# Kernel tuning notes

Measured on AMD Instinct MI355X. Metric: run time of the kernel, lower is better.

The kernel has to match this reference:

```python
import jax, jax.numpy as jnp
import numpy as np


def _conv1x1_relu(x, W, b):
    # x: (B, Cin, N, k), W: (Cout, Cin), b: (Cout,) -> (B, Cout, N, k)
    return jax.nn.relu(jnp.einsum('bcnk,oc->bonk', x, W) + b[None, :, None, None])


def _knn_idx(pc, k):
    # pc: (B, C, N). Mirrors torch: dis_mat = -||pi - pj||^2, topk (largest) -> nearest.
    G = jnp.einsum('bcn,bcm->bnm', pc, pc)            # (B, N, N)
    sq = jnp.sum(pc * pc, axis=1)                      # (B, N)
    neg_dist = 2.0 * G - sq[:, :, None] - sq[:, None, :]
    _, idx = jax.lax.top_k(neg_dist, k)                # (B, N, k) int32
    return idx


def _group_points(x, idx):
    # x: (B, C, N), idx: (B, N, k) -> (B, C, N, k); out[b,c,n,j] = x[b,c,idx[b,n,j]]
    B, C, N = x.shape
    k = idx.shape[-1]
    idx2 = jnp.broadcast_to(idx.reshape(B, 1, N * k), (B, C, N * k))
    return jnp.take_along_axis(x, idx2, axis=2).reshape(B, C, N, k)


def setup_inputs() -> dict:
    key = jax.random.key(0)
    ks = jax.random.split(key, 8)
    B, N, C, O, K = 8, 4096, 64, 64, 16
    s = 0.05
    return {
        'xyz': jax.random.normal(ks[0], (B, 3, N), dtype=jnp.float32),
        'fea': jax.random.normal(ks[1], (B, C, N), dtype=jnp.float32),
        'Wg1': jax.random.normal(ks[2], (O, 10), dtype=jnp.float32) * s,
        'bg1': jnp.zeros((O,), dtype=jnp.float32),
        'Wg2': jax.random.normal(ks[3], (O, O), dtype=jnp.float32) * s,
        'bg2': jnp.zeros((O,), dtype=jnp.float32),
        'Wf1': jax.random.normal(ks[4], (O, 2 * C), dtype=jnp.float32) * s,
        'bf1': jnp.zeros((O,), dtype=jnp.float32),
        'Wf2': jax.random.normal(ks[5], (O, O), dtype=jnp.float32) * s,
        'bf2': jnp.zeros((O,), dtype=jnp.float32),
        'Wf3': jax.random.normal(ks[6], (O, O), dtype=jnp.float32) * s,
        'bf3': jnp.zeros((O,), dtype=jnp.float32),
        'k': 16,
    }


def reference(xyz, fea, Wg1, bg1, Wg2, bg2, Wf1, bf1, Wf2, bf2, Wf3, bf3, k):
    idx = _knn_idx(fea, k)                             # (B, N, k)

    # get_edge_point: (B, 10, N, k)
    xyz_knn = _group_points(xyz, idx)                  # (B, 3, N, k)
    xyz_c = jnp.broadcast_to(xyz[:, :, :, None], xyz_knn.shape)
    xyz_r = xyz_c - xyz_knn
    xyz_d = jnp.sqrt(jnp.sum(xyz_r * xyz_r, axis=1, keepdims=True))
    geo = jnp.concatenate([xyz_d, xyz_c, xyz_knn, xyz_r], axis=1)

    # get_edge_feature: (B, 2C, N, k)
    fea_knn = _group_points(fea, idx)
    fea_c = jnp.broadcast_to(fea[:, :, :, None], fea_knn.shape)
    edge = jnp.concatenate([fea_c, fea_knn], axis=1)

    g = _conv1x1_relu(geo, Wg1, bg1)
    g = _conv1x1_relu(g, Wg2, bg2)

    f = _conv1x1_relu(edge, Wf1, bf1)
    f = _conv1x1_relu(f, Wf2, bf2)
    f = _conv1x1_relu(f, Wf3, bf3)

    out = jnp.max(g * f, axis=-1)                      # (B, O, N)
    return out
```

## Files before the change

### kernel.cpp

```cpp
#include <hip/hip_runtime.h>
#include <math.h>

#define NB 8
#define NPTS 4096
#define NCH 64
#define NOUT 64
#define KNN 16

#define GLOBAL_AS const __attribute__((address_space(1)))
#define LDS_AS __attribute__((address_space(3)))

#define WS_SQ  0
#define WS_PT  (NB*NPTS)
#define WS_QT  (WS_PT + NB*NPTS*64)
#define WS_IDX (WS_QT + NB*NPTS*64)

__global__ __launch_bounds__(256) void k_sq(const float* __restrict__ fea,
                                            float* __restrict__ sq) {
    int g = blockIdx.x * 256 + threadIdx.x;
    int b = g >> 12, n = g & 4095;
    const float* f = fea + (size_t)b * NCH * NPTS + n;
    float s = 0.f;
#pragma unroll
    for (int c = 0; c < NCH; ++c) s = fmaf(f[c * NPTS], f[c * NPTS], s);
    sq[g] = s;
}

__global__ __launch_bounds__(256, 2) void k_knn(const float* __restrict__ fea,
                                                const float* __restrict__ sq,
                                                int* __restrict__ idxout) {
    __shared__ __align__(16) float rowT[64][64];
    __shared__ __align__(16) float colT[2][64 * 64];
    __shared__ __align__(16) float D[64 * 64];

    const int b = blockIdx.y;
    const int n0 = blockIdx.x * 64;
    const int tid = threadIdx.x;
    const int to = tid & 15, tp = tid >> 4;
    const int lane = tid & 63, w = tid >> 6;
    const int g = lane >> 4, p = lane & 15;
    const int wbase = w * 16;
    const float* feab = fea + (size_t)b * NCH * NPTS;

    auto stage_async = [&](int buf, int m0) {
#pragma unroll
        for (int i = 0; i < 4; ++i) {
            int k = w * 4 + i;
            int c = 4 * k + (lane >> 4);
            int j = (lane & 15) * 4;
            const float* gp = feab + c * NPTS + m0 + j;
            float* lp = &colT[buf][k * 256];
            __builtin_amdgcn_global_load_lds((GLOBAL_AS void*)gp,
                                             (LDS_AS void*)lp, 16, 0, 0);
        }
    };

#pragma unroll
    for (int i = 0; i < 4; ++i) {
        int e = i * 1024 + tid * 4;
        int c = e >> 6, r = e & 63;
        *(float4*)&rowT[c][r] = *(const float4*)&feab[c * NPTS + n0 + r];
    }
    stage_async(0, 0);

    float lstv[4];
    int   lsti[4];
#pragma unroll
    for (int i = 0; i < 4; ++i) { lstv[i] = -3.0e38f; lsti[i] = 0; }

    auto ins = [&](int i, float vv, int col) {
        unsigned long long lt = __ballot(lstv[i] < vv);
        int pos = __popc((unsigned)((lt >> (g * 16)) & 0xFFFFull));
        float nv = __shfl_down(lstv[i], 1, 16);
        int   ni = __shfl_down(lsti[i], 1, 16);
        if (p <= pos - 2)      { lstv[i] = nv; lsti[i] = ni; }
        else if (p == pos - 1) { lstv[i] = vv; lsti[i] = col; }
    };

    __syncthreads();

    for (int t = 0; t < 64; ++t) {
        const int m0 = t * 64;
        const int cur = t & 1;
        if (t < 63) stage_async(cur ^ 1, m0 + 64);

        float4 sqc = *(const float4*)&sq[b * NPTS + m0 + tp * 4];

        float acc[4][4] = {{0.f,0.f,0.f,0.f},{0.f,0.f,0.f,0.f},
                           {0.f,0.f,0.f,0.f},{0.f,0.f,0.f,0.f}};
#pragma unroll 8
        for (int c = 0; c < 64; ++c) {
            float4 rv = *(const float4*)&rowT[c][to * 4];
            float4 cv = *(const float4*)&colT[cur][c * 64 + tp * 4];
            float rr[4] = {rv.x, rv.y, rv.z, rv.w};
            float cc[4] = {cv.x, cv.y, cv.z, cv.w};
#pragma unroll
            for (int ri = 0; ri < 4; ++ri)
#pragma unroll
                for (int ci = 0; ci < 4; ++ci)
                    acc[ri][ci] = fmaf(rr[ri], cc[ci], acc[ri][ci]);
        }

        float sqa[4] = {sqc.x, sqc.y, sqc.z, sqc.w};
#pragma unroll
        for (int ri = 0; ri < 4; ++ri) {
            int row = to * 4 + ri;
            int colp = (tp * 4) ^ (((row >> 2) & 15) << 2);
            float4 o;
            o.x = 2.f * acc[ri][0] - sqa[0];
            o.y = 2.f * acc[ri][1] - sqa[1];
            o.z = 2.f * acc[ri][2] - sqa[2];
            o.w = 2.f * acc[ri][3] - sqa[3];
            *(float4*)&D[row * 64 + colp] = o;
        }
        asm volatile("s_waitcnt lgkmcnt(0)\n\ts_barrier" ::: "memory");

        float4 dv[4];
        float thr[4];
#pragma unroll
        for (int i = 0; i < 4; ++i) {
            int row = wbase + g * 4 + i;
            int swz = ((row >> 2) & 15) << 2;
            dv[i] = *(const float4*)&D[row * 64 + ((p * 4) ^ swz)];
            thr[i] = __shfl(lstv[i], 0, 16);
        }
#pragma unroll
        for (int i = 0; i < 4; ++i) {
            float vm = fmaxf(fmaxf(dv[i].x, dv[i].y), fmaxf(dv[i].z, dv[i].w));
            unsigned long long bal = __ballot(vm > thr[i]);
            unsigned mg = (unsigned)((bal >> (g * 16)) & 0xFFFFull);
            while (__any(mg != 0u)) {
                bool act = (mg != 0u);
                int srcp = act ? (__ffs(mg) - 1) : 0;
                mg &= (mg - 1u);
                int srcl = (g << 4) | srcp;
                float c0 = __shfl(dv[i].x, srcl);
                float c1 = __shfl(dv[i].y, srcl);
                float c2 = __shfl(dv[i].z, srcl);
                float c3 = __shfl(dv[i].w, srcl);
                if (act) {
                    int cb = m0 + srcp * 4;
                    if (c0 > thr[i]) ins(i, c0, cb + 0);
                    if (c1 > thr[i]) ins(i, c1, cb + 1);
                    if (c2 > thr[i]) ins(i, c2, cb + 2);
                    if (c3 > thr[i]) ins(i, c3, cb + 3);
                }
            }
        }
        __syncthreads();
    }

#pragma unroll
    for (int i = 0; i < 4; ++i) {
        int row = wbase + g * 4 + i;
        idxout[((size_t)(b * NPTS) + n0 + row) * KNN + (15 - p)] = lsti[i];
    }
}

__global__ __launch_bounds__(256) void k_pq(const float* __restrict__ fea,
                                            const float* __restrict__ Wf1,
                                            const float* __restrict__ bf1,
                                            float* __restrict__ Pt,
                                            float* __restrict__ Qt) {
    __shared__ __align__(16) float feaT[64][64];
    __shared__ __align__(16) float WT[64][132];
    __shared__ float sb[64];

    const int b = blockIdx.y;
    const int n0 = blockIdx.x * 64;
    const int tid = threadIdx.x;
    const int to = tid & 15, tn = tid >> 4;
    const float* feab = fea + (size_t)b * NCH * NPTS;

#pragma unroll
    for (int i = 0; i < 4; ++i) {
        int e = i * 1024 + tid * 4;
        int c = e >> 6, nn = e & 63;
        *(float4*)&feaT[c][nn] = *(const float4*)&feab[c * NPTS + n0 + nn];
    }
#pragma unroll
    for (int i = 0; i < 8; ++i) {
        int g = tid * 32 + i * 4;
        int op = g >> 6, c = g & 63;
        const float* src = (op < 64) ? &Wf1[op * 128 + c]
                                     : &Wf1[(op - 64) * 128 + 64 + c];
        float4 w = *(const float4*)src;
        WT[c + 0][op] = w.x; WT[c + 1][op] = w.y;
        WT[c + 2][op] = w.z; WT[c + 3][op] = w.w;
    }
    if (tid < 64) sb[tid] = bf1[tid];
    __syncthreads();

    float acc[4][8];
#pragma unroll
    for (int ni = 0; ni < 4; ++ni)
#pragma unroll
        for (int oj = 0; oj < 8; ++oj) acc[ni][oj] = 0.f;

#pragma unroll 4
    for (int c = 0; c < 64; ++c) {
        float4 a  = *(const float4*)&feaT[c][tn * 4];
        float4 w0 = *(const float4*)&WT[c][to * 8];
        float4 w1 = *(const float4*)&WT[c][to * 8 + 4];
        float av[4] = {a.x, a.y, a.z, a.w};
        float wv[8] = {w0.x, w0.y, w0.z, w0.w, w1.x, w1.y, w1.z, w1.w};
#pragma unroll
        for (int ni = 0; ni < 4; ++ni)
#pragma unroll
            for (int oj = 0; oj < 8; ++oj)
                acc[ni][oj] = fmaf(av[ni], wv[oj], acc[ni][oj]);
    }

    const int opb = to * 8;
#pragma unroll
    for (int ni = 0; ni < 4; ++ni) {
        int n = n0 + tn * 4 + ni;
        size_t base = ((size_t)b * NPTS + n) * 64;
        if (opb < 64) {
            float4 o0, o1;
            o0.x = acc[ni][0] + sb[opb + 0]; o0.y = acc[ni][1] + sb[opb + 1];
            o0.z = acc[ni][2] + sb[opb + 2]; o0.w = acc[ni][3] + sb[opb + 3];
            o1.x = acc[ni][4] + sb[opb + 4]; o1.y = acc[ni][5] + sb[opb + 5];
            o1.z = acc[ni][6] + sb[opb + 6]; o1.w = acc[ni][7] + sb[opb + 7];
            *(float4*)&Pt[base + opb]     = o0;
            *(float4*)&Pt[base + opb + 4] = o1;
        } else {
            float4 o0, o1;
            o0.x = acc[ni][0]; o0.y = acc[ni][1]; o0.z = acc[ni][2]; o0.w = acc[ni][3];
            o1.x = acc[ni][4]; o1.y = acc[ni][5]; o1.z = acc[ni][6]; o1.w = acc[ni][7];
            *(float4*)&Qt[base + opb - 64]     = o0;
            *(float4*)&Qt[base + opb - 64 + 4] = o1;
        }
    }
}

__global__ __launch_bounds__(256) void k_mlp(
    const float* __restrict__ xyz,
    const float* __restrict__ Pt, const float* __restrict__ Qt,
    const int* __restrict__ knnidx,
    const float* __restrict__ Wg1, const float* __restrict__ bg1,
    const float* __restrict__ Wg2, const float* __restrict__ bg2,
    const float* __restrict__ Wf2, const float* __restrict__ bf2,
    const float* __restrict__ Wf3, const float* __restrict__ bf3,
    float* __restrict__ out) {
    __shared__ __align__(16) float bufX[64][68];
    __shared__ __align__(16) float bufY[64][68];
    __shared__ __align__(16) float Wbuf[64][68];
    __shared__ __align__(16) float scratch[1280];
    __shared__ float biasS[64];
    __shared__ int sidx[64];

    const int b = blockIdx.y;
    const int n0 = blockIdx.x * 4;
    const int tid = threadIdx.x;
    const int to = tid & 15, tp = tid >> 4;

    if (tid < 64)
        sidx[tid] = knnidx[((size_t)(b * NPTS + n0)) * KNN + tid];
    __syncthreads();

    {
        int pair = tid >> 2, q = tid & 3;
        int m = sidx[pair];
        int pt = pair >> 4;
        const float* pB = &Pt[((size_t)b * NPTS + n0 + pt) * 64];
        const float* qB = &Qt[((size_t)b * NPTS + m) * 64];
#pragma unroll
        for (int i = 0; i < 4; ++i) {
            int c0 = q * 16 + i * 4;
            float4 pv = *(const float4*)&pB[c0];
            float4 qv = *(const float4*)&qB[c0];
            bufX[c0 + 0][pair] = fmaxf(pv.x + qv.x, 0.f);
            bufX[c0 + 1][pair] = fmaxf(pv.y + qv.y, 0.f);
            bufX[c0 + 2][pair] = fmaxf(pv.z + qv.z, 0.f);
            bufX[c0 + 3][pair] = fmaxf(pv.w + qv.w, 0.f);
        }
    }
    if (tid < 64) {
        int pair = tid, pt = pair >> 4;
        int m = sidx[pair];
        const float* xb = xyz + (size_t)b * 3 * NPTS;
        float cx = xb[0 * NPTS + n0 + pt], cy = xb[1 * NPTS + n0 + pt], cz = xb[2 * NPTS + n0 + pt];
        float kx = xb[0 * NPTS + m], ky = xb[1 * NPTS + m], kz = xb[2 * NPTS + m];
        float rx = cx - kx, ry = cy - ky, rz = cz - kz;
        float d = sqrtf(rx * rx + ry * ry + rz * rz);
        scratch[0 * 68 + pair] = d;
        scratch[1 * 68 + pair] = cx; scratch[2 * 68 + pair] = cy; scratch[3 * 68 + pair] = cz;
        scratch[4 * 68 + pair] = kx; scratch[5 * 68 + pair] = ky; scratch[6 * 68 + pair] = kz;
        scratch[7 * 68 + pair] = rx; scratch[8 * 68 + pair] = ry; scratch[9 * 68 + pair] = rz;
    }

    auto stageW = [&](const float* W, const float* bv) {
#pragma unroll
        for (int i = 0; i < 4; ++i) {
            int g = tid * 16 + i * 4;
            int o = g >> 6, c = g & 63;
            float4 w = *(const float4*)&W[g];
            Wbuf[c + 0][o] = w.x; Wbuf[c + 1][o] = w.y;
            Wbuf[c + 2][o] = w.z; Wbuf[c + 3][o] = w.w;
        }
        if (tid < 64) biasS[tid] = bv[tid];
    };

    auto gemmPh = [&](const float* src, float* dst, int Kdim) {
        float acc[4][4] = {{0.f,0.f,0.f,0.f},{0.f,0.f,0.f,0.f},
                           {0.f,0.f,0.f,0.f},{0.f,0.f,0.f,0.f}};
#pragma unroll 2
        for (int c = 0; c < Kdim; ++c) {
            float4 w = *(const float4*)&Wbuf[c][to * 4];
            float4 a = *(const float4*)(src + c * 68 + tp * 4);
            float wr[4] = {w.x, w.y, w.z, w.w};
            float ar[4] = {a.x, a.y, a.z, a.w};
#pragma unroll
            for (int oi = 0; oi < 4; ++oi)
#pragma unroll
                for (int pj = 0; pj < 4; ++pj)
                    acc[oi][pj] = fmaf(wr[oi], ar[pj], acc[oi][pj]);
        }
#pragma unroll
        for (int oi = 0; oi < 4; ++oi) {
            float bo = biasS[to * 4 + oi];
            float4 o4;
            o4.x = fmaxf(acc[oi][0] + bo, 0.f);
            o4.y = fmaxf(acc[oi][1] + bo, 0.f);
            o4.z = fmaxf(acc[oi][2] + bo, 0.f);
            o4.w = fmaxf(acc[oi][3] + bo, 0.f);
            *(float4*)(dst + (to * 4 + oi) * 68 + tp * 4) = o4;
        }
    };

    stageW(Wf2, bf2);
    __syncthreads();
    gemmPh(&bufX[0][0], &bufY[0][0], 64);
    __syncthreads();
    stageW(Wf3, bf3);
    __syncthreads();
    gemmPh(&bufY[0][0], &bufX[0][0], 64);
    __syncthreads();
    {
        for (int e = tid; e < 640; e += 256) {
            int o = e / 10, c = e - o * 10;
            Wbuf[c][o] = Wg1[e];
        }
        if (tid < 64) biasS[tid] = bg1[tid];
    }
    __syncthreads();
    gemmPh(scratch, &bufY[0][0], 10);
    __syncthreads();
    stageW(Wg2, bg2);
    __syncthreads();
    {
        float acc[4][4] = {{0.f,0.f,0.f,0.f},{0.f,0.f,0.f,0.f},
                           {0.f,0.f,0.f,0.f},{0.f,0.f,0.f,0.f}};
#pragma unroll 2
        for (int c = 0; c < 64; ++c) {
            float4 w = *(const float4*)&Wbuf[c][to * 4];
            float4 a = *(const float4*)&bufY[c][tp * 4];
            float wr[4] = {w.x, w.y, w.z, w.w};
            float ar[4] = {a.x, a.y, a.z, a.w};
#pragma unroll
            for (int oi = 0; oi < 4; ++oi)
#pragma unroll
                for (int pj = 0; pj < 4; ++pj)
                    acc[oi][pj] = fmaf(wr[oi], ar[pj], acc[oi][pj]);
        }
#pragma unroll
        for (int oi = 0; oi < 4; ++oi) {
            int o = to * 4 + oi;
            float bo = biasS[o];
            float mx = -3.0e38f;
#pragma unroll
            for (int pj = 0; pj < 4; ++pj) {
                float g2v = fmaxf(acc[oi][pj] + bo, 0.f);
                float f3v = bufX[o][tp * 4 + pj];
                mx = fmaxf(mx, g2v * f3v);
            }
            scratch[o * 17 + tp] = mx;
        }
    }
    __syncthreads();
    {
        int o = tid & 63, pt = tid >> 6;
        float m0_ = scratch[o * 17 + pt * 4 + 0];
        float m1  = scratch[o * 17 + pt * 4 + 1];
        float m2  = scratch[o * 17 + pt * 4 + 2];
        float m3  = scratch[o * 17 + pt * 4 + 3];
        out[((size_t)b * 64 + o) * NPTS + n0 + pt] =
            fmaxf(fmaxf(m0_, m1), fmaxf(m2, m3));
    }
}

extern "C" void kernel_launch(void* const* d_in, const int* in_sizes, int n_in,
                              void* d_out, int out_size, void* d_ws, size_t ws_size,
                              hipStream_t stream) {
    const float* xyz = (const float*)d_in[0];
    const float* fea = (const float*)d_in[1];
    const float* Wg1 = (const float*)d_in[2];
    const float* bg1 = (const float*)d_in[3];
    const float* Wg2 = (const float*)d_in[4];
    const float* bg2 = (const float*)d_in[5];
    const float* Wf1 = (const float*)d_in[6];
    const float* bf1 = (const float*)d_in[7];
    const float* Wf2 = (const float*)d_in[8];
    const float* bf2 = (const float*)d_in[9];
    const float* Wf3 = (const float*)d_in[10];
    const float* bf3 = (const float*)d_in[11];
    float* out = (float*)d_out;
    float* ws = (float*)d_ws;

    float* sq = ws + WS_SQ;
    float* Pt = ws + WS_PT;
    float* Qt = ws + WS_QT;
    int* idxw = (int*)(ws + WS_IDX);

    k_sq <<<dim3(128),      dim3(256), 0, stream>>>(fea, sq);
    k_knn<<<dim3(64, 8),    dim3(256), 0, stream>>>(fea, sq, idxw);
    k_pq <<<dim3(64, 8),    dim3(256), 0, stream>>>(fea, Wf1, bf1, Pt, Qt);
    k_mlp<<<dim3(1024, 8),  dim3(256), 0, stream>>>(xyz, Pt, Qt, idxw,
                                                    Wg1, bg1, Wg2, bg2,
                                                    Wf2, bf2, Wf3, bf3, out);
}
```

Measured before the change: 759.2 us.

## Remap KNN GEMM thread tile so selection reads accumulators directly

Changes the thread-to-output mapping of the 64x64 distance tile so each thread computes the same rows and columns it later scans in the top-k selection. This removes the shared-memory D staging buffer, its swizzled writes and reads, and one barrier per tile iteration. It also frees LDS, which could allow more resident blocks. The trade-off is that the rowT reads become broadcast-heavy within each 16-lane group, and the LDS access pattern changes.

Result: faster. 737.1 us (-2.9%).

```diff
diff --git a/kernel.cpp b/kernel.cpp
--- a/kernel.cpp
+++ b/kernel.cpp
@@ -31,15 +31,13 @@
                                                 int* __restrict__ idxout) {
     __shared__ __align__(16) float rowT[64][64];
     __shared__ __align__(16) float colT[2][64 * 64];
-    __shared__ __align__(16) float D[64 * 64];
 
     const int b = blockIdx.y;
     const int n0 = blockIdx.x * 64;
     const int tid = threadIdx.x;
-    const int to = tid & 15, tp = tid >> 4;
     const int lane = tid & 63, w = tid >> 6;
     const int g = lane >> 4, p = lane & 15;
-    const int wbase = w * 16;
+    const int rbase = w * 16 + g * 4;
     const float* feab = fea + (size_t)b * NCH * NPTS;
 
     auto stage_async = [&](int buf, int m0) {
@@ -84,14 +82,14 @@
         const int cur = t & 1;
         if (t < 63) stage_async(cur ^ 1, m0 + 64);
 
-        float4 sqc = *(const float4*)&sq[b * NPTS + m0 + tp * 4];
+        float4 sqc = *(const float4*)&sq[b * NPTS + m0 + p * 4];
 
         float acc[4][4] = {{0.f,0.f,0.f,0.f},{0.f,0.f,0.f,0.f},
                            {0.f,0.f,0.f,0.f},{0.f,0.f,0.f,0.f}};
 #pragma unroll 8
         for (int c = 0; c < 64; ++c) {
-            float4 rv = *(const float4*)&rowT[c][to * 4];
-            float4 cv = *(const float4*)&colT[cur][c * 64 + tp * 4];
+            float4 rv = *(const float4*)&rowT[c][rbase];
+            float4 cv = *(const float4*)&colT[cur][c * 64 + p * 4];
             float rr[4] = {rv.x, rv.y, rv.z, rv.w};
             float cc[4] = {cv.x, cv.y, cv.z, cv.w};
 #pragma unroll
@@ -101,32 +99,20 @@
                     acc[ri][ci] = fmaf(rr[ri], cc[ci], acc[ri][ci]);
         }
 
-        float sqa[4] = {sqc.x, sqc.y, sqc.z, sqc.w};
-#pragma unroll
-        for (int ri = 0; ri < 4; ++ri) {
-            int row = to * 4 + ri;
-            int colp = (tp * 4) ^ (((row >> 2) & 15) << 2);
-            float4 o;
-            o.x = 2.f * acc[ri][0] - sqa[0];
-            o.y = 2.f * acc[ri][1] - sqa[1];
-            o.z = 2.f * acc[ri][2] - sqa[2];
-            o.w = 2.f * acc[ri][3] - sqa[3];
-            *(float4*)&D[row * 64 + colp] = o;
-        }
-        asm volatile("s_waitcnt lgkmcnt(0)\n\ts_barrier" ::: "memory");
-
-        float4 dv[4];
         float thr[4];
 #pragma unroll
         for (int i = 0; i < 4; ++i) {
-            int row = wbase + g * 4 + i;
-            int swz = ((row >> 2) & 15) << 2;
-            dv[i] = *(const float4*)&D[row * 64 + ((p * 4) ^ swz)];
+            acc[i][0] = 2.f * acc[i][0] - sqc.x;
+            acc[i][1] = 2.f * acc[i][1] - sqc.y;
+            acc[i][2] = 2.f * acc[i][2] - sqc.z;
+            acc[i][3] = 2.f * acc[i][3] - sqc.w;
             thr[i] = __shfl(lstv[i], 0, 16);
         }
+
 #pragma unroll
         for (int i = 0; i < 4; ++i) {
-            float vm = fmaxf(fmaxf(dv[i].x, dv[i].y), fmaxf(dv[i].z, dv[i].w));
+            float vm = fmaxf(fmaxf(acc[i][0], acc[i][1]),
+                             fmaxf(acc[i][2], acc[i][3]));
             unsigned long long bal = __ballot(vm > thr[i]);
             unsigned mg = (unsigned)((bal >> (g * 16)) & 0xFFFFull);
             while (__any(mg != 0u)) {
@@ -134,10 +120,10 @@
                 int srcp = act ? (__ffs(mg) - 1) : 0;
                 mg &= (mg - 1u);
                 int srcl = (g << 4) | srcp;
-                float c0 = __shfl(dv[i].x, srcl);
-                float c1 = __shfl(dv[i].y, srcl);
-                float c2 = __shfl(dv[i].z, srcl);
-                float c3 = __shfl(dv[i].w, srcl);
+                float c0 = __shfl(acc[i][0], srcl);
+                float c1 = __shfl(acc[i][1], srcl);
+                float c2 = __shfl(acc[i][2], srcl);
+                float c3 = __shfl(acc[i][3], srcl);
                 if (act) {
                     int cb = m0 + srcp * 4;
                     if (c0 > thr[i]) ins(i, c0, cb + 0);
@@ -152,7 +138,7 @@
 
 #pragma unroll
     for (int i = 0; i < 4; ++i) {
-        int row = wbase + g * 4 + i;
+        int row = rbase + i;
         idxout[((size_t)(b * NPTS) + n0 + row) * KNN + (15 - p)] = lsti[i];
     }
 }
```
